# Optimization experiments

Measured on AMD Instinct MI355X. Metric: run time of the kernel, lower is better.

## Reference

```python
import jax, jax.numpy as jnp
import numpy as np

VOCAB = 50257
D_MODEL = 1024
PAD_IDX = 0
B, L = 4, 4096


def setup_inputs() -> dict:
    key = jax.random.key(0)
    k1, k2, k3, k4, k5 = jax.random.split(key, 5)
    input_ids = jax.random.randint(k1, (B, L), 0, VOCAB, dtype=jnp.int64 if jax.config.jax_enable_x64 else jnp.int32)
    role_mask = jax.random.randint(k2, (B, L), 0, 2, dtype=input_ids.dtype)
    emb = jax.random.normal(k3, (VOCAB, D_MODEL), dtype=jnp.float32)
    emb = emb.at[PAD_IDX].set(0.0)  # padding_idx row is zero in nn.Embedding
    # nn.Linear weight has shape (out, in); y = x @ W.T
    scale = 1.0 / np.sqrt(D_MODEL)
    W0 = jax.random.uniform(k4, (D_MODEL, D_MODEL), dtype=jnp.float32, minval=-scale, maxval=scale)
    W1 = jax.random.uniform(k5, (D_MODEL, D_MODEL), dtype=jnp.float32, minval=-scale, maxval=scale)
    return {"input_ids": input_ids, "role_mask": role_mask, "emb": emb, "W0": W0, "W1": W1}


def reference(input_ids, role_mask, emb, W0, W1):
    # Embedding lookup: (B, L, D)
    x = emb[input_ids]
    # Per-role linear transform (2-expert routing); compute both, select by mask.
    y0 = jnp.einsum('bld,ed->ble', x, W0)
    y1 = jnp.einsum('bld,ed->ble', x, W1)
    out = jnp.where((role_mask == 1)[..., None], y1, y0)
    return out
```

## Files before the change

kernel.cpp:

```cpp
#include <hip/hip_runtime.h>


#define M_TOK   16384
#define DIM     1024
#define MT      128
#define NTIL    130
#define XROWS   (NTIL * MT)
#define BK      64
#define PBLK    64
#define WBLKS   2048

typedef __attribute__((ext_vector_type(8))) short short8;
typedef __attribute__((ext_vector_type(4))) float f32x4;

#define OFF_PERM 256
#define OFF_WB   66816
#define OFF_X    4261120

static __device__ __forceinline__ unsigned short f2bf(float f) {
    unsigned int u = __float_as_uint(f);
    u += 0x7fffu + ((u >> 16) & 1u);
    return (unsigned short)(u >> 16);
}

__global__ void k_pre(const int* __restrict__ role, int* perm, int* cnt,
                      const float* __restrict__ W0, const float* __restrict__ W1,
                      unsigned short* __restrict__ Wb) {
    int b = blockIdx.x;
    if (b < PBLK) {
        int t = b * 256 + threadIdx.x;
        int row;
        if (role[t] == 1) { int s = atomicAdd(&cnt[1], 1); row = XROWS - 1 - s; }
        else              { int s = atomicAdd(&cnt[0], 1); row = s; }
        perm[row] = t;
    } else {
        int idx = ((b - PBLK) * 256 + threadIdx.x) * 4;
        const float* src = (idx < 1048576) ? (W0 + idx) : (W1 + (idx - 1048576));
        float4 f = *(const float4*)src;
        *(ushort4*)(Wb + idx) = make_ushort4(f2bf(f.x), f2bf(f.y), f2bf(f.z), f2bf(f.w));
    }
}

__global__ void k_gather(const int* __restrict__ ids, const int* __restrict__ perm,
                         const int* __restrict__ cnt, const float* __restrict__ emb,
                         unsigned short* __restrict__ X) {
    int b = blockIdx.x;
    int n0 = cnt[0], n1 = cnt[1];
    if (b >= n0 && b < XROWS - n1) return;
    int p = perm[b];
    int id = ids[p];
    int t = threadIdx.x;
    float4 f = *(const float4*)(emb + (size_t)id * DIM + t * 4);
    *(ushort4*)(X + (size_t)b * DIM + t * 4) =
        make_ushort4(f2bf(f.x), f2bf(f.y), f2bf(f.z), f2bf(f.w));
}

__global__ __launch_bounds__(256, 3)
void k_gemm(const unsigned short* __restrict__ Xu, const unsigned short* __restrict__ Wbu,
            const int* __restrict__ perm, const int* __restrict__ cnt,
            float* __restrict__ out) {
    __shared__ short As[MT * BK];
    __shared__ short Bs[MT * BK];

    int f  = blockIdx.x;
    int mt = ((f >> 6) << 3) | (f & 7);
    int nt = (f >> 3) & 7;
    if (mt >= NTIL) return;

    int n0 = cnt[0], n1 = cnt[1];
    int T0 = (n0 + 127) >> 7, T1 = (n1 + 127) >> 7;
    int e, lo, hi;
    if (mt < T0)              { e = 0; lo = 0;            hi = n0;    }
    else if (mt >= NTIL - T1) { e = 1; lo = XROWS - n1;   hi = XROWS; }
    else return;

    const short* Ag = (const short*)Xu + (size_t)mt * MT * DIM;
    const short* Bg = (const short*)Wbu + (size_t)e * DIM * DIM + (size_t)nt * MT * DIM;

    int tid  = threadIdx.x;
    int lane = tid & 63;
    int w    = tid >> 6;
    int wm   = w & 1, wn = w >> 1;
    int quad = lane >> 4, lq = lane & 15;

    f32x4 acc[4][4] = {};

    for (int k0 = 0; k0 < DIM; k0 += BK) {
#pragma unroll
        for (int i = 0; i < 4; ++i) {
            int q   = w * 4 + i;
            int s   = q * 64 + lane;
            int row = s >> 3;
            int kc  = (s & 7) ^ (row & 7);
            __builtin_amdgcn_global_load_lds(
                (const __attribute__((address_space(1))) unsigned int*)(Ag + (size_t)row * DIM + k0 + kc * 8),
                (__attribute__((address_space(3))) unsigned int*)(&As[s * 8]),
                16, 0, 0);
            __builtin_amdgcn_global_load_lds(
                (const __attribute__((address_space(1))) unsigned int*)(Bg + (size_t)row * DIM + k0 + kc * 8),
                (__attribute__((address_space(3))) unsigned int*)(&Bs[s * 8]),
                16, 0, 0);
        }
        __syncthreads();

#pragma unroll
        for (int s = 0; s < 2; ++s) {
            short8 av[4], bv[4];
            int s4q = s * 4 + quad;
#pragma unroll
            for (int i = 0; i < 4; ++i) {
                int ra = wm * 64 + i * 16 + lq;
                av[i] = *(const short8*)&As[(ra * 8 + (s4q ^ (ra & 7))) * 8];
                int rb = wn * 64 + i * 16 + lq;
                bv[i] = *(const short8*)&Bs[(rb * 8 + (s4q ^ (rb & 7))) * 8];
            }
#pragma unroll
            for (int i = 0; i < 4; ++i)
#pragma unroll
                for (int j = 0; j < 4; ++j)
                    acc[i][j] = __builtin_amdgcn_mfma_f32_16x16x32_bf16(
                        av[i], bv[j], acc[i][j], 0, 0, 0);
        }
        __syncthreads();
    }

    int colbase = nt * 128 + wn * 64 + lq;
#pragma unroll
    for (int i = 0; i < 4; ++i) {
#pragma unroll
        for (int r = 0; r < 4; ++r) {
            int mrow = mt * MT + wm * 64 + i * 16 + quad * 4 + r;
            if (mrow < lo || mrow >= hi) continue;
            int token = perm[mrow];
            float* o = out + (size_t)token * DIM + colbase;
#pragma unroll
            for (int j = 0; j < 4; ++j)
                o[j * 16] = acc[i][j][r];
        }
    }
}

extern "C" void kernel_launch(void* const* d_in, const int* in_sizes, int n_in,
                              void* d_out, int out_size, void* d_ws, size_t ws_size,
                              hipStream_t stream) {
    const int*   ids  = (const int*)d_in[0];
    const int*   role = (const int*)d_in[1];
    const float* emb  = (const float*)d_in[2];
    const float* W0   = (const float*)d_in[3];
    const float* W1   = (const float*)d_in[4];
    float*       out  = (float*)d_out;

    char* ws = (char*)d_ws;
    int* cnt  = (int*)ws;
    int* perm = (int*)(ws + OFF_PERM);
    unsigned short* Wb = (unsigned short*)(ws + OFF_WB);
    unsigned short* X  = (unsigned short*)(ws + OFF_X);

    hipMemsetAsync(cnt, 0x00, 2 * sizeof(int), stream);
    k_pre   <<<PBLK + WBLKS, 256, 0, stream>>>(role, perm, cnt, W0, W1, Wb);
    k_gather<<<XROWS,        256, 0, stream>>>(ids, perm, cnt, emb, X);
    k_gemm  <<<1088,         256, 0, stream>>>(X, Wb, perm, cnt, out);
}
```

Before: 331.2 us.

## Fuse memset, routing, weight cast and gather into one cooperative kernel

Replaces the memset plus the two pre-GEMM kernels with a single cooperative kernel. It uses grid.sync to order counter reset, token routing, weight conversion and embedding gather. Routing now uses wave ballots and block-level aggregation, so each block issues one global atomic per role instead of one per token. This saves launch gaps and atomic contention, but adds grid-wide barriers and a persistent-grid loop over rows that may balance load less evenly.

```diff
diff --git a/kernel.cpp b/kernel.cpp
--- a/kernel.cpp
+++ b/kernel.cpp
@@ -1,4 +1,7 @@
 #include <hip/hip_runtime.h>
+#include <hip/hip_cooperative_groups.h>
+
+namespace cg = cooperative_groups;
 
 
 #define M_TOK   16384
@@ -7,8 +10,7 @@
 #define NTIL    130
 #define XROWS   (NTIL * MT)
 #define BK      64
-#define PBLK    64
-#define WBLKS   2048
+#define NB      1024
 
 typedef __attribute__((ext_vector_type(8))) short short8;
 typedef __attribute__((ext_vector_type(4))) float f32x4;
@@ -23,36 +25,66 @@
     return (unsigned short)(u >> 16);
 }
 
-__global__ void k_pre(const int* __restrict__ role, int* perm, int* cnt,
+__global__ void k_pre(const int* __restrict__ role, const int* __restrict__ ids,
+                      const float* __restrict__ emb,
                       const float* __restrict__ W0, const float* __restrict__ W1,
-                      unsigned short* __restrict__ Wb) {
-    int b = blockIdx.x;
-    if (b < PBLK) {
-        int t = b * 256 + threadIdx.x;
-        int row;
-        if (role[t] == 1) { int s = atomicAdd(&cnt[1], 1); row = XROWS - 1 - s; }
-        else              { int s = atomicAdd(&cnt[0], 1); row = s; }
-        perm[row] = t;
+                      int* perm, int* cnt,
+                      unsigned short* __restrict__ Wb, unsigned short* __restrict__ X) {
+    cg::grid_group grid = cg::this_grid();
+    __shared__ int lc[2];
+    __shared__ int wbase[4][2];
+    __shared__ int gbase[2];
+
+    int b = blockIdx.x, t = threadIdx.x;
+
+    if (b == 0 && t < 2) cnt[t] = 0;
+    grid.sync();
+
+    if (b < 64) {
+        int tok = b * 256 + t;
+        int r = (role[tok] == 1) ? 1 : 0;
+        if (t < 2) lc[t] = 0;
+        __syncthreads();
+        int wv = t >> 6, lane = t & 63;
+        unsigned long long m = __ballot(r);
+        int c1 = __popcll(m);
+        unsigned long long lower = m & ((1ull << lane) - 1ull);
+        int rank1 = __popcll(lower);
+        int rank0 = lane - rank1;
+        if (lane == 0) {
+            wbase[wv][1] = atomicAdd(&lc[1], c1);
+            wbase[wv][0] = atomicAdd(&lc[0], 64 - c1);
+        }
+        __syncthreads();
+        if (t == 0) {
+            gbase[0] = atomicAdd(&cnt[0], lc[0]);
+            gbase[1] = atomicAdd(&cnt[1], lc[1]);
+        }
+        __syncthreads();
+        int idx = r ? (gbase[1] + wbase[wv][1] + rank1)
+                    : (gbase[0] + wbase[wv][0] + rank0);
+        int row = r ? (XROWS - 1 - idx) : idx;
+        perm[row] = tok;
     } else {
-        int idx = ((b - PBLK) * 256 + threadIdx.x) * 4;
-        const float* src = (idx < 1048576) ? (W0 + idx) : (W1 + (idx - 1048576));
-        float4 f = *(const float4*)src;
-        *(ushort4*)(Wb + idx) = make_ushort4(f2bf(f.x), f2bf(f.y), f2bf(f.z), f2bf(f.w));
+        for (int i = (b - 64) * 256 + t; i < 524288; i += (NB - 64) * 256) {
+            int idx = i * 4;
+            const float* src = (idx < 1048576) ? (W0 + idx) : (W1 + (idx - 1048576));
+            float4 f = *(const float4*)src;
+            *(ushort4*)(Wb + idx) =
+                make_ushort4(f2bf(f.x), f2bf(f.y), f2bf(f.z), f2bf(f.w));
+        }
     }
-}
+    grid.sync();
 
-__global__ void k_gather(const int* __restrict__ ids, const int* __restrict__ perm,
-                         const int* __restrict__ cnt, const float* __restrict__ emb,
-                         unsigned short* __restrict__ X) {
-    int b = blockIdx.x;
     int n0 = cnt[0], n1 = cnt[1];
-    if (b >= n0 && b < XROWS - n1) return;
-    int p = perm[b];
-    int id = ids[p];
-    int t = threadIdx.x;
-    float4 f = *(const float4*)(emb + (size_t)id * DIM + t * 4);
-    *(ushort4*)(X + (size_t)b * DIM + t * 4) =
-        make_ushort4(f2bf(f.x), f2bf(f.y), f2bf(f.z), f2bf(f.w));
+    for (int row = b; row < XROWS; row += NB) {
+        if (row >= n0 && row < XROWS - n1) continue;
+        int p  = perm[row];
+        int id = ids[p];
+        float4 f = *(const float4*)(emb + (size_t)id * DIM + t * 4);
+        *(ushort4*)(X + (size_t)row * DIM + t * 4) =
+            make_ushort4(f2bf(f.x), f2bf(f.y), f2bf(f.z), f2bf(f.w));
+    }
 }
 
 __global__ __launch_bounds__(256, 3)
@@ -156,8 +188,8 @@
     unsigned short* Wb = (unsigned short*)(ws + OFF_WB);
     unsigned short* X  = (unsigned short*)(ws + OFF_X);
 
-    hipMemsetAsync(cnt, 0x00, 2 * sizeof(int), stream);
-    k_pre   <<<PBLK + WBLKS, 256, 0, stream>>>(role, perm, cnt, W0, W1, Wb);
-    k_gather<<<XROWS,        256, 0, stream>>>(ids, perm, cnt, emb, X);
-    k_gemm  <<<1088,         256, 0, stream>>>(X, Wb, perm, cnt, out);
+    void* args[] = { (void*)&role, (void*)&ids, (void*)&emb, (void*)&W0, (void*)&W1,
+                     (void*)&perm, (void*)&cnt, (void*)&Wb, (void*)&X };
+    hipLaunchCooperativeKernel((const void*)k_pre, dim3(NB), dim3(256), args, 0, stream);
+    k_gemm<<<1088, 256, 0, stream>>>(X, Wb, perm, cnt, out);
 }
```

Result: slower. 565.2 us (+70.7%).
